# Performance work log

Measured on AMD Instinct MI355X. Metric: run time of the kernel, lower is better.

The kernel has to match this reference:

```python
import jax, jax.numpy as jnp
import numpy as np

MODES = 20
WIDTH = 64
EPS = 1e-5


def spectral_conv(x, w1, w2, m1, m2):
    # x: [B, C, H, W] real; w1, w2: [Ci, Co, m1, m2, 2] (real/imag)
    B, C, H, W = x.shape
    xf = jnp.fft.rfft2(x, norm='ortho')  # [B, C, H, W//2+1] complex
    w1c = w1[..., 0] + 1j * w1[..., 1]
    w2c = w2[..., 0] + 1j * w2[..., 1]
    m1 = min(m1, H)
    m2 = min(m2, W // 2 + 1)
    top = jnp.einsum('bixy,ioxy->boxy', xf[:, :, :m1, :m2], w1c[:, :, :m1, :m2])
    bot = jnp.einsum('bixy,ioxy->boxy', xf[:, :, -m1:, :m2], w2c[:, :, :m1, :m2])
    out = jnp.zeros((B, w1.shape[1], H, W // 2 + 1), dtype=xf.dtype)
    out = out.at[:, :, :m1, :m2].set(top)
    out = out.at[:, :, H - m1:, :m2].set(bot)
    return jnp.fft.irfft2(out, s=(H, W), norm='ortho')


def batchnorm2d(x, gamma, beta):
    # training-mode BN over (B, H, W) per channel; x: [B, C, H, W]
    mean = jnp.mean(x, axis=(0, 2, 3), keepdims=True)
    var = jnp.var(x, axis=(0, 2, 3), keepdims=True)
    xn = (x - mean) * jax.lax.rsqrt(var + EPS)
    return xn * gamma[None, :, None, None] + beta[None, :, None, None]


def setup_inputs() -> dict:
    key = jax.random.key(0)
    ks = jax.random.split(key, 12)
    B, H, W, Tin2 = 8, 256, 256, 12
    scale = 1.0 / (WIDTH * WIDTH)
    return {
        'x': jax.random.normal(ks[0], (B, H, W, Tin2), jnp.float32),
        'fc0_w': jax.random.normal(ks[1], (Tin2, WIDTH), jnp.float32) * 0.1,
        'fc0_b': jnp.zeros((WIDTH,), jnp.float32),
        'sw1': scale * jax.random.normal(ks[2], (4, WIDTH, WIDTH, MODES, MODES, 2), jnp.float32),
        'sw2': scale * jax.random.normal(ks[3], (4, WIDTH, WIDTH, MODES, MODES, 2), jnp.float32),
        'cw': jax.random.normal(ks[4], (4, WIDTH, WIDTH), jnp.float32) * 0.1,
        'cb': jnp.zeros((4, WIDTH), jnp.float32),
        'bng': jnp.ones((4, WIDTH), jnp.float32),
        'bnb': jnp.zeros((4, WIDTH), jnp.float32),
        'fc1_w': jax.random.normal(ks[5], (WIDTH, 128), jnp.float32) * 0.1,
        'fc1_b': jnp.zeros((128,), jnp.float32),
        'fc2_w': jax.random.normal(ks[6], (128, 1), jnp.float32) * 0.1,
        'fc2_b': jnp.zeros((1,), jnp.float32),
    }


def reference(x, fc0_w, fc0_b, sw1, sw2, cw, cb, bng, bnb, fc1_w, fc1_b, fc2_w, fc2_b):
    # lift: [B, H, W, Tin+2] -> [B, C, H, W]
    h = jnp.einsum('bhwt,tc->bhwc', x, fc0_w) + fc0_b
    h = jnp.transpose(h, (0, 3, 1, 2))
    for l in range(4):
        spec = spectral_conv(h, sw1[l], sw2[l], MODES, MODES)
        lin = jnp.einsum('bihw,oi->bohw', h, cw[l]) + cb[l][None, :, None, None]
        h = batchnorm2d(spec + lin, bng[l], bnb[l])
        if l < 3:
            h = jax.nn.relu(h)
    h = jnp.transpose(h, (0, 2, 3, 1))  # [B, H, W, C]
    h = jax.nn.relu(jnp.einsum('bhwc,cd->bhwd', h, fc1_w) + fc1_b)
    out = jnp.einsum('bhwd,de->bhwe', h, fc2_w) + fc2_b
    return out
```

## Files before the change

### kernel.cpp

```cpp
#include <hip/hip_runtime.h>
#include <hip/hip_bf16.h>


__device__ __forceinline__ void gll16(const float* gsrc, float* ldst) {
    __builtin_amdgcn_global_load_lds(
        (const __attribute__((address_space(1))) void*)gsrc,
        (__attribute__((address_space(3))) void*)ldst, 16, 0, 0);
}

__global__ __launch_bounds__(256) void init_k(const float* __restrict__ cw,
                                              float* __restrict__ costab, float* __restrict__ sintab,
                                              float* __restrict__ EAt, float* __restrict__ Tw,
                                              float* __restrict__ cwT, float* __restrict__ stats) {
    int idx = blockIdx.x * 256 + threadIdx.x;
    const float PH = 6.28318530717958647692f / 256.f;
    if (idx < 256) {
        float s, c; sincosf(idx * PH, &s, &c);
        costab[idx] = c; sintab[idx] = s;
    } else if (idx < 256 + 10240) {
        int e = idx - 256;
        int n = e >> 8, w = e & 255, ky = n >> 1;
        int r = (ky * w) & 255;
        float s, c; sincosf(r * PH, &s, &c);
        EAt[e] = (n & 1) ? -s : c;
    } else if (idx < 256 + 20480) {
        int e = idx - 10496;
        int kp = e >> 8, w = e & 255;
        int ky = kp >> 1, p = kp & 1;
        int r = (ky * w) & 255;
        float s, c; sincosf(r * PH, &s, &c);
        float v;
        if (ky == 0) v = p ? 0.f : (1.f / 16.f);
        else         v = p ? (-2.f / 16.f) * s : (2.f / 16.f) * c;
        Tw[e] = v;
    } else if (idx < 256 + 20480 + 16384) {
        int e = idx - 20736;
        int l = e >> 12, r2 = e & 4095;
        int i = r2 >> 6, o = r2 & 63;
        cwT[e] = cw[(l << 12) + (o << 6) + i];
    } else if (idx < 256 + 20480 + 16384 + 2048) {
        stats[idx - 37120] = 0.f;
    }
}

__global__ __launch_bounds__(256) void wtrans_k(const float* __restrict__ sw1,
                                                const float* __restrict__ sw2,
                                                unsigned int* __restrict__ wt) {
    int gid = blockIdx.x * 4 + (threadIdx.x >> 6);
    int o = threadIdx.x & 63;
    int xyc = gid % 25;
    int i = (gid / 25) & 63;
    int t2 = gid / 1600;
    const float* src = ((t2 & 1) ? sw2 : sw1) + (t2 >> 1) * 3276800;
    const float* sp = src + ((i * 64 + o) * 400 + xyc * 16) * 2;
    unsigned int* dp = wt + (size_t)(t2 * 400 + xyc * 16) * 4096 + i * 64 + o;
#pragma unroll
    for (int j = 0; j < 16; ++j) {
        float re = sp[2 * j], im = sp[2 * j + 1];
        unsigned int ur = __float_as_uint(re), ui = __float_as_uint(im);
        ur = (ur + 0x7fffu + ((ur >> 16) & 1u)) >> 16;
        ui = (ui + 0x7fffu + ((ui >> 16) & 1u)) & 0xffff0000u;
        dp[(size_t)j * 4096] = ur | ui;
    }
}

__global__ __launch_bounds__(256) void fc0_k(const float* __restrict__ x,
                                             const float* __restrict__ w,
                                             const float* __restrict__ bias,
                                             float* __restrict__ outb) {
    __shared__ float ws[768];
    __shared__ float bs[64];
    int tid = threadIdx.x;
    for (int i = tid; i < 768; i += 256) ws[i] = w[i];
    if (tid < 64) bs[tid] = bias[tid];
    __syncthreads();
    int pix = blockIdx.x * 256 + tid;
    int b = pix >> 16, hw = pix & 65535;
    float xv[12];
#pragma unroll
    for (int t = 0; t < 12; ++t) xv[t] = x[pix * 12 + t];
    int base = (b << 22) + hw;
    for (int c = 0; c < 64; ++c) {
        float a = bs[c];
#pragma unroll
        for (int t = 0; t < 12; ++t) a += xv[t] * ws[t * 64 + c];
        outb[base + (c << 16)] = a;
    }
}

__global__ __launch_bounds__(128) void dftw_k(float* __restrict__ X,
                                              const float* __restrict__ EAt,
                                              float* __restrict__ T,
                                              const float* __restrict__ statsl,
                                              const float* __restrict__ g,
                                              const float* __restrict__ bt,
                                              int fuse) {
    __shared__ __align__(16) float Xs[32 * 68];
    __shared__ __align__(16) float Est[40 * 32];
    int tid = threadIdx.x;
    int tm = tid >> 3, tn = tid & 7;
    int row0 = blockIdx.x << 6;
    float sc = 1.f, sh = 0.f;
    if (fuse) {
        int c = (row0 >> 8) & 63;
        float ssum = statsl[c] + statsl[128 + c] + statsl[256 + c] + statsl[384 + c];
        float ssq  = statsl[64 + c] + statsl[192 + c] + statsl[320 + c] + statsl[448 + c];
        float mean = ssum * (1.f / 524288.f);
        float var = ssq * (1.f / 524288.f) - mean * mean;
        sc = g[c] * rsqrtf(var + 1e-5f);
        sh = bt[c] - mean * sc;
    }
    float acc[4][5];
#pragma unroll
    for (int i = 0; i < 4; ++i)
#pragma unroll
        for (int j = 0; j < 5; ++j) acc[i][j] = 0.f;

#pragma unroll 1
    for (int kc = 0; kc < 256; kc += 32) {
        __syncthreads();
#pragma unroll
        for (int r = 0; r < 4; ++r) {
            int m = tm + (r << 4);
            float4 v = *(const float4*)&X[(row0 + m) * 256 + kc + (tn << 2)];
            if (fuse) {
                v.x = fmaxf(fmaf(v.x, sc, sh), 0.f);
                v.y = fmaxf(fmaf(v.y, sc, sh), 0.f);
                v.z = fmaxf(fmaf(v.z, sc, sh), 0.f);
                v.w = fmaxf(fmaf(v.w, sc, sh), 0.f);
                *(float4*)&X[(row0 + m) * 256 + kc + (tn << 2)] = v;
            }
            int kb = tn << 2;
            Xs[(kb + 0) * 68 + m] = v.x;
            Xs[(kb + 1) * 68 + m] = v.y;
            Xs[(kb + 2) * 68 + m] = v.z;
            Xs[(kb + 3) * 68 + m] = v.w;
        }
        for (int i = tid; i < 1280; i += 128) Est[i] = EAt[((i >> 5) << 8) + kc + (i & 31)];
        __syncthreads();
#pragma unroll 1
        for (int k4 = 0; k4 < 8; ++k4) {
            float4 e0 = *(const float4*)&Est[(tn * 5 + 0) * 32 + (k4 << 2)];
            float4 e1 = *(const float4*)&Est[(tn * 5 + 1) * 32 + (k4 << 2)];
            float4 e2 = *(const float4*)&Est[(tn * 5 + 2) * 32 + (k4 << 2)];
            float4 e3 = *(const float4*)&Est[(tn * 5 + 3) * 32 + (k4 << 2)];
            float4 e4 = *(const float4*)&Est[(tn * 5 + 4) * 32 + (k4 << 2)];
#pragma unroll
            for (int c2 = 0; c2 < 4; ++c2) {
                float4 a = *(const float4*)&Xs[((k4 << 2) + c2) * 68 + (tm << 2)];
                float ev0 = ((const float*)&e0)[c2];
                float ev1 = ((const float*)&e1)[c2];
                float ev2 = ((const float*)&e2)[c2];
                float ev3 = ((const float*)&e3)[c2];
                float ev4 = ((const float*)&e4)[c2];
                acc[0][0] += a.x * ev0; acc[1][0] += a.y * ev0; acc[2][0] += a.z * ev0; acc[3][0] += a.w * ev0;
                acc[0][1] += a.x * ev1; acc[1][1] += a.y * ev1; acc[2][1] += a.z * ev1; acc[3][1] += a.w * ev1;
                acc[0][2] += a.x * ev2; acc[1][2] += a.y * ev2; acc[2][2] += a.z * ev2; acc[3][2] += a.w * ev2;
                acc[0][3] += a.x * ev3; acc[1][3] += a.y * ev3; acc[2][3] += a.z * ev3; acc[3][3] += a.w * ev3;
                acc[0][4] += a.x * ev4; acc[1][4] += a.y * ev4; acc[2][4] += a.z * ev4; acc[3][4] += a.w * ev4;
            }
        }
    }
#pragma unroll
    for (int i = 0; i < 4; ++i) {
        int row = row0 + (tm << 2) + i;
#pragma unroll
        for (int j = 0; j < 5; ++j) T[row * 40 + tn * 5 + j] = acc[i][j];
    }
}

__global__ __launch_bounds__(256) void dfth_k(const float* __restrict__ T,
                                              const float* __restrict__ ct, const float* __restrict__ st,
                                              float* __restrict__ XF) {
    __shared__ __align__(16) float Ts[10240];
    __shared__ float cts[256], sts[256];
    int tid = threadIdx.x;
    int bc = blockIdx.x;
    for (int i = tid; i < 10240; i += 256) Ts[i] = T[bc * 10240 + i];
    cts[tid] = ct[tid]; sts[tid] = st[tid];
    __syncthreads();
    if (tid < 200) {
        int kxi = tid / 5, kyg = tid % 5;
        int kxa = kxi < 20 ? kxi : kxi + 216;
        float ar0 = 0, ai0 = 0, ar1 = 0, ai1 = 0, ar2 = 0, ai2 = 0, ar3 = 0, ai3 = 0;
        int r = 0;
#pragma unroll 1
        for (int h = 0; h < 256; ++h) {
            float cc = cts[r], sv = sts[r];
            r = (r + kxa) & 255;
            float4 v0 = *(const float4*)&Ts[h * 40 + (kyg << 3)];
            float4 v1 = *(const float4*)&Ts[h * 40 + (kyg << 3) + 4];
            ar0 += v0.x * cc + v0.y * sv;  ai0 += v0.y * cc - v0.x * sv;
            ar1 += v0.z * cc + v0.w * sv;  ai1 += v0.w * cc - v0.z * sv;
            ar2 += v1.x * cc + v1.y * sv;  ai2 += v1.y * cc - v1.x * sv;
            ar3 += v1.z * cc + v1.w * sv;  ai3 += v1.w * cc - v1.z * sv;
        }
        int b = bc >> 6, c = bc & 63;
        const float s = 1.f / 256.f;
        int A = (b * 40 + kxi) * 20 + (kyg << 2);
        float2* O = (float2*)XF;
        O[(A + 0) * 64 + c] = make_float2(ar0 * s, ai0 * s);
        O[(A + 1) * 64 + c] = make_float2(ar1 * s, ai1 * s);
        O[(A + 2) * 64 + c] = make_float2(ar2 * s, ai2 * s);
        O[(A + 3) * 64 + c] = make_float2(ar3 * s, ai3 * s);
    }
}

__global__ __launch_bounds__(512) void eins_t_k(const float* __restrict__ XF,
                                                const unsigned int* __restrict__ wtl,
                                                float* __restrict__ YF) {
    __shared__ float xfs[1024];
    int tid = threadIdx.x;
    int x = blockIdx.x / 20, y = blockIdx.x % 20;
    for (int i = tid; i < 1024; i += 512) {
        int b = i >> 7, rr = i & 127;
        xfs[i] = XF[(b * 40 + x) * 2560 + y * 128 + rr];
    }
    __syncthreads();
    int b = tid >> 6, o = tid & 63;
    const unsigned int* wp = wtl + (size_t)(((x < 20 ? 0 : 400) + (x % 20) * 20 + y)) * 4096 + o;
    float ar = 0.f, ai = 0.f;
#pragma unroll 8
    for (int i = 0; i < 64; ++i) {
        unsigned int wv = wp[i << 6];
        float wr = __uint_as_float(wv << 16);
        float wi = __uint_as_float(wv & 0xffff0000u);
        float xr = xfs[(b << 7) + (i << 1)];
        float xi = xfs[(b << 7) + (i << 1) + 1];
        ar += xr * wr - xi * wi;
        ai += xr * wi + xi * wr;
    }
    ((float2*)YF)[((b * 40 + x) * 20 + y) * 64 + o] = make_float2(ar, ai);
}

__global__ __launch_bounds__(512) void eins_k(const float* __restrict__ XF,
                                              const float* __restrict__ w1, const float* __restrict__ w2,
                                              float* __restrict__ YF) {
    __shared__ float xfs[1024];
    int tid = threadIdx.x;
    int x = blockIdx.x / 20, y = blockIdx.x % 20;
    for (int i = tid; i < 1024; i += 512) {
        int b = i >> 7, rr = i & 127;
        xfs[i] = XF[(b * 40 + x) * 2560 + y * 128 + rr];
    }
    __syncthreads();
    int b = tid >> 6, o = tid & 63;
    const float* wp = (x < 20) ? (w1 + (x * 20 + y) * 2) : (w2 + ((x - 20) * 20 + y) * 2);
    float ar = 0.f, ai = 0.f;
#pragma unroll 8
    for (int i = 0; i < 64; ++i) {
        float2 wv = *(const float2*)&wp[(i * 64 + o) * 800];
        float xr = xfs[(b << 7) + (i << 1)];
        float xi = xfs[(b << 7) + (i << 1) + 1];
        ar += xr * wv.x - xi * wv.y;
        ai += xr * wv.y + xi * wv.x;
    }
    ((float2*)YF)[((b * 40 + x) * 20 + y) * 64 + o] = make_float2(ar, ai);
}

__global__ __launch_bounds__(256) void idfth_k(const float* __restrict__ YF,
                                               const float* __restrict__ ct, const float* __restrict__ st,
                                               float* __restrict__ Z) {
    __shared__ __align__(16) float yfs[1600];
    __shared__ float cts[256], sts[256];
    int tid = threadIdx.x;
    int bc = blockIdx.x;
    int b = bc >> 6, co = bc & 63;
    for (int i = tid; i < 800; i += 256) {
        int kx = i / 20, ky = i % 20;
        float2 v = ((const float2*)YF)[((b * 40 + kx) * 20 + ky) * 64 + co];
        yfs[kx * 40 + 2 * ky] = v.x;
        yfs[kx * 40 + 2 * ky + 1] = v.y;
    }
    cts[tid] = ct[tid]; sts[tid] = st[tid];
    __syncthreads();
    int h = tid;
    float accr[20], acci[20];
#pragma unroll
    for (int q = 0; q < 20; ++q) { accr[q] = 0.f; acci[q] = 0.f; }
#pragma unroll 1
    for (int kxi = 0; kxi < 40; ++kxi) {
        int kxa = kxi < 20 ? kxi : kxi + 216;
        int r = (kxa * h) & 255;
        float cc = cts[r], sv = sts[r];
#pragma unroll
        for (int q = 0; q < 10; ++q) {
            float4 v = *(const float4*)&yfs[kxi * 40 + (q << 2)];
            accr[2 * q]     += v.x * cc - v.y * sv;  acci[2 * q]     += v.x * sv + v.y * cc;
            accr[2 * q + 1] += v.z * cc - v.w * sv;  acci[2 * q + 1] += v.z * sv + v.w * cc;
        }
    }
    const float s = 1.f / 16.f;
    int base = (bc * 256 + h) * 40;
#pragma unroll
    for (int q = 0; q < 10; ++q) {
        float4 o4;
        o4.x = accr[2 * q] * s;     o4.y = acci[2 * q] * s;
        o4.z = accr[2 * q + 1] * s; o4.w = acci[2 * q + 1] * s;
        *(float4*)&Z[base + (q << 2)] = o4;
    }
}

#define FMA2(I, AV, J, B4) \
    acc[I][J].x += (AV) * B4.x; acc[I][J].y += (AV) * B4.y; \
    acc[I][J].z += (AV) * B4.z; acc[I][J].w += (AV) * B4.w;

#define FMA_COL(J, B4) \
    FMA2(0, a0.x, J, B4) FMA2(1, a0.y, J, B4) FMA2(2, a0.z, J, B4) FMA2(3, a0.w, J, B4) \
    FMA2(4, a1.x, J, B4) FMA2(5, a1.y, J, B4) FMA2(6, a1.z, J, B4) FMA2(7, a1.w, J, B4)

#define FMA_COLU(J, B4) \
    FMA2(0, au0.x, J, B4) FMA2(1, au0.y, J, B4) FMA2(2, au0.z, J, B4) FMA2(3, au0.w, J, B4) \
    FMA2(4, au1.x, J, B4) FMA2(5, au1.y, J, B4) FMA2(6, au1.z, J, B4) FMA2(7, au1.w, J, B4)

#define FMA_COLD(J, B4) \
    FMA2(0, ad0.x, J, B4) FMA2(1, ad0.y, J, B4) FMA2(2, ad0.z, J, B4) FMA2(3, ad0.w, J, B4) \
    FMA2(4, ad1.x, J, B4) FMA2(5, ad1.y, J, B4) FMA2(6, ad1.z, J, B4) FMA2(7, ad1.w, J, B4)

__global__ __launch_bounds__(256) void speclin_k(const float* __restrict__ hin,
                                                 const float* __restrict__ Z,
                                                 const float* __restrict__ cwTl,
                                                 const float* __restrict__ Tw,
                                                 const float* __restrict__ cbl,
                                                 float* __restrict__ pre,
                                                 float* __restrict__ statsl) {
    __shared__ __align__(16) float As[64 * 68];
    __shared__ __align__(16) float Zs[80 * 64];
    __shared__ __align__(16) float Bs[2][4096];
    int tid = threadIdx.x;
    int bid = blockIdx.x;
    int b = bid >> 7, hp = bid & 127;
    int h0 = hp << 1;
    int to = tid >> 5, tw = tid & 31;
    int o0 = to << 3;

#pragma unroll
    for (int t = 0; t < 4; ++t) {
        int i4 = tid + (t << 8);
        float4 v = *(const float4*)&cwTl[i4 << 2];
        float* d = &As[(i4 >> 4) * 68 + ((i4 & 15) << 2)];
        d[0] = v.x; d[1] = v.y; d[2] = v.z; d[3] = v.w;
    }
#pragma unroll
    for (int t = 0; t < 5; ++t) {
        int i4 = tid + (t << 8);
        int q = i4 % 10;
        int u = i4 / 10;
        int o = u & 63, r = u >> 6;
        float4 v = *(const float4*)&Z[(((b << 6) + o) * 256 + h0 + r) * 40 + (q << 2)];
        int base = ((r * 40 + (q << 2)) << 6) + o;
        Zs[base]       = v.x;
        Zs[base + 64]  = v.y;
        Zs[base + 128] = v.z;
        Zs[base + 192] = v.w;
    }
    const float* hrow = hin + (size_t)((((b << 6) << 8) + h0) << 8);
#pragma unroll
    for (int t = 0; t < 4; ++t) {
        int i4 = tid + (t << 8);
        int k = i4 >> 7, n4 = i4 & 127, r = n4 >> 6, w4 = n4 & 63;
        gll16(&hrow[(k << 16) + (r << 8) + (w4 << 2)], &Bs[0][i4 << 2]);
    }
    __syncthreads();

    float4 acc[8][4];
#pragma unroll
    for (int i = 0; i < 8; ++i)
#pragma unroll
        for (int j = 0; j < 4; ++j) acc[i][j] = make_float4(0.f, 0.f, 0.f, 0.f);

    int cur = 0;
#pragma unroll 1
    for (int ch = 0; ch < 8; ++ch) {
        if (ch < 7) {
#pragma unroll
            for (int t = 0; t < 4; ++t) {
                int i4 = tid + (t << 8);
                int k = i4 >> 7, n4 = i4 & 127, r = n4 >> 6, w4 = n4 & 63;
                gll16(&hrow[((((ch + 1) << 3) + k) << 16) + (r << 8) + (w4 << 2)],
                      &Bs[cur ^ 1][i4 << 2]);
            }
        } else {
#pragma unroll
            for (int t = 0; t < 2; ++t) {
                int i4 = tid + (t << 8);
                gll16(&Tw[i4 << 2], &Bs[cur ^ 1][i4 << 2]);
            }
        }
        const float* Bc = Bs[cur];
        const float* Ac = &As[(ch << 3) * 68 + o0];
#pragma unroll 1
        for (int kk = 0; kk < 8; ++kk) {
            float4 a0 = *(const float4*)&Ac[kk * 68];
            float4 a1 = *(const float4*)&Ac[kk * 68 + 4];
            float4 b0 = *(const float4*)&Bc[(kk << 9) + (tw << 2)];
            float4 b1 = *(const float4*)&Bc[(kk << 9) + 128 + (tw << 2)];
            FMA_COL(0, b0)
            FMA_COL(1, b1)
            float4 b2 = *(const float4*)&Bc[(kk << 9) + 256 + (tw << 2)];
            float4 b3 = *(const float4*)&Bc[(kk << 9) + 384 + (tw << 2)];
            FMA_COL(2, b2)
            FMA_COL(3, b3)
        }
        __syncthreads();
        cur ^= 1;
    }

#pragma unroll 1
    for (int ch = 0; ch < 5; ++ch) {
        if (ch < 4) {
#pragma unroll
            for (int t = 0; t < 2; ++t) {
                int i4 = tid + (t << 8);
                gll16(&Tw[(((ch + 1) << 3) << 8) + (i4 << 2)], &Bs[cur ^ 1][i4 << 2]);
            }
        }
        const float* Bc = Bs[cur];
#pragma unroll 1
        for (int kk = 0; kk < 8; ++kk) {
            int kp = (ch << 3) + kk;
            float4 b0 = *(const float4*)&Bc[(kk << 8) + (tw << 2)];
            float4 b1 = *(const float4*)&Bc[(kk << 8) + 128 + (tw << 2)];
            float4 au0 = *(const float4*)&Zs[(kp << 6) + o0];
            float4 au1 = *(const float4*)&Zs[(kp << 6) + o0 + 4];
            FMA_COLU(0, b0)
            FMA_COLU(1, b1)
            float4 ad0 = *(const float4*)&Zs[((40 + kp) << 6) + o0];
            float4 ad1 = *(const float4*)&Zs[((40 + kp) << 6) + o0 + 4];
            FMA_COLD(2, b0)
            FMA_COLD(3, b1)
        }
        __syncthreads();
        cur ^= 1;
    }

    float* srep = statsl + ((bid & 3) << 7);
#pragma unroll
    for (int i = 0; i < 8; ++i) {
        float cbv = cbl[o0 + i];
        float sum = 0.f, sq = 0.f;
#pragma unroll
        for (int j = 0; j < 4; ++j) {
            float4 v = acc[i][j];
            v.x += cbv; v.y += cbv; v.z += cbv; v.w += cbv;
            int row = h0 + (j >> 1);
            int wc = ((j & 1) << 7) + (tw << 2);
            *(float4*)&pre[(size_t)((((b << 6) + o0 + i) << 8) + row) * 256 + wc] = v;
            sum += v.x + v.y + v.z + v.w;
            sq  += v.x * v.x + v.y * v.y + v.z * v.z + v.w * v.w;
        }
        sum += __shfl_xor(sum, 1);  sq += __shfl_xor(sq, 1);
        sum += __shfl_xor(sum, 2);  sq += __shfl_xor(sq, 2);
        sum += __shfl_xor(sum, 4);  sq += __shfl_xor(sq, 4);
        sum += __shfl_xor(sum, 8);  sq += __shfl_xor(sq, 8);
        sum += __shfl_xor(sum, 16); sq += __shfl_xor(sq, 16);
        if ((tid & 31) == 0) {
            atomicAdd(&srep[o0 + i], sum);
            atomicAdd(&srep[64 + o0 + i], sq);
        }
    }
}

__global__ __launch_bounds__(256, 2) void fc12_k(const float* __restrict__ hin,
                                                 const float* __restrict__ statsl,
                                                 const float* __restrict__ g,
                                                 const float* __restrict__ bt,
                                                 const float* __restrict__ w1, const float* __restrict__ b1,
                                                 const float* __restrict__ w2, const float* __restrict__ b2,
                                                 float* __restrict__ out) {
    __shared__ __align__(16) float As[64 * 128];
    __shared__ __align__(16) float Bs[2][2048];
    __shared__ float scs[64], shs[64], bias2[128];
    __shared__ __align__(16) float red[4 * 256];
    int tid = threadIdx.x;
    int bh = blockIdx.x;
    int b = bh >> 8, h = bh & 255;
    int to = tid >> 4, tw = tid & 15;
    int d0 = to << 3;

    if (tid < 64) {
        float ssum = statsl[tid] + statsl[128 + tid] + statsl[256 + tid] + statsl[384 + tid];
        float ssq  = statsl[64 + tid] + statsl[192 + tid] + statsl[320 + tid] + statsl[448 + tid];
        float mean = ssum * (1.f / 524288.f);
        float var = ssq * (1.f / 524288.f) - mean * mean;
        float s = g[tid] * rsqrtf(var + 1e-5f);
        scs[tid] = s; shs[tid] = bt[tid] - mean * s;
    }
    __syncthreads();
    for (int i = tid; i < 8192; i += 256) As[i] = w1[i] * scs[i >> 7];
    if (tid < 128) {
        float a = b1[tid];
        for (int c = 0; c < 64; ++c) a += shs[c] * w1[c * 128 + tid];
        bias2[tid] = a;
    }
    const float* hrow = hin + ((size_t)(((b << 6) << 8) + h) << 8);
#pragma unroll
    for (int t = 0; t < 2; ++t) {
        int i4 = tid + (t << 8);
        gll16(&hrow[((i4 >> 6) << 16) + ((i4 & 63) << 2)], &Bs[0][i4 << 2]);
    }
    __syncthreads();

    float4 acc[8][4];
#pragma unroll
    for (int i = 0; i < 8; ++i)
#pragma unroll
        for (int j = 0; j < 4; ++j) acc[i][j] = make_float4(0.f, 0.f, 0.f, 0.f);

    int cur = 0;
#pragma unroll 1
    for (int ch = 0; ch < 8; ++ch) {
        if (ch < 7) {
#pragma unroll
            for (int t = 0; t < 2; ++t) {
                int i4 = tid + (t << 8);
                int k = i4 >> 6, w4 = (i4 & 63) << 2;
                gll16(&hrow[((((ch + 1) << 3) + k) << 16) + w4], &Bs[cur ^ 1][i4 << 2]);
            }
        }
        const float* Bc = Bs[cur];
#pragma unroll 2
        for (int kk = 0; kk < 8; ++kk) {
            int gk = (ch << 3) + kk;
            float4 a0 = *(const float4*)&As[(gk << 7) + d0];
            float4 a1 = *(const float4*)&As[(gk << 7) + d0 + 4];
            float4 b0 = *(const float4*)&Bc[(kk << 8) + (tw << 2)];
            float4 b1 = *(const float4*)&Bc[(kk << 8) + 64 + (tw << 2)];
            FMA_COL(0, b0)
            FMA_COL(1, b1)
            float4 b2 = *(const float4*)&Bc[(kk << 8) + 128 + (tw << 2)];
            float4 b3 = *(const float4*)&Bc[(kk << 8) + 192 + (tw << 2)];
            FMA_COL(2, b2)
            FMA_COL(3, b3)
        }
        __syncthreads();
        cur ^= 1;
    }

    float bb[8], wv[8];
#pragma unroll
    for (int i = 0; i < 8; ++i) { bb[i] = bias2[d0 + i]; wv[i] = w2[d0 + i]; }
    float4 p[4];
#pragma unroll
    for (int j = 0; j < 4; ++j) {
        float4 v = make_float4(0.f, 0.f, 0.f, 0.f);
#pragma unroll
        for (int i = 0; i < 8; ++i) {
            v.x += fmaxf(acc[i][j].x + bb[i], 0.f) * wv[i];
            v.y += fmaxf(acc[i][j].y + bb[i], 0.f) * wv[i];
            v.z += fmaxf(acc[i][j].z + bb[i], 0.f) * wv[i];
            v.w += fmaxf(acc[i][j].w + bb[i], 0.f) * wv[i];
        }
        v.x += __shfl_xor(v.x, 16); v.y += __shfl_xor(v.y, 16);
        v.z += __shfl_xor(v.z, 16); v.w += __shfl_xor(v.w, 16);
        v.x += __shfl_xor(v.x, 32); v.y += __shfl_xor(v.y, 32);
        v.z += __shfl_xor(v.z, 32); v.w += __shfl_xor(v.w, 32);
        p[j] = v;
    }
    int wave = tid >> 6;
    if ((tid & 63) < 16) {
#pragma unroll
        for (int j = 0; j < 4; ++j)
            *(float4*)&red[(wave << 8) + (j << 6) + (tw << 2)] = p[j];
    }
    __syncthreads();
    float s2 = b2[0] + red[tid] + red[256 + tid] + red[512 + tid] + red[768 + tid];
    out[(b * 256 + h) * 256 + tid] = s2;
}

extern "C" void kernel_launch(void* const* d_in, const int* in_sizes, int n_in,
                              void* d_out, int out_size, void* d_ws, size_t ws_size,
                              hipStream_t stream) {
    (void)in_sizes; (void)n_in; (void)out_size;
    const float* x     = (const float*)d_in[0];
    const float* fc0_w = (const float*)d_in[1];
    const float* fc0_b = (const float*)d_in[2];
    const float* sw1   = (const float*)d_in[3];
    const float* sw2   = (const float*)d_in[4];
    const float* cw    = (const float*)d_in[5];
    const float* cb    = (const float*)d_in[6];
    const float* bng   = (const float*)d_in[7];
    const float* bnb   = (const float*)d_in[8];
    const float* fc1_w = (const float*)d_in[9];
    const float* fc1_b = (const float*)d_in[10];
    const float* fc2_w = (const float*)d_in[11];
    const float* fc2_b = (const float*)d_in[12];
    float* out = (float*)d_out;

    float* ws = (float*)d_ws;
    float* hbuf   = ws;
    float* tz     = hbuf + 33554432;
    float* xf     = tz + 5242880;
    float* yf     = xf + 819200;
    float* costab = yf + 819200;
    float* sintab = costab + 256;
    float* EAt    = sintab + 256;
    float* Tw     = EAt + 10240;
    float* cwT    = Tw + 10240;
    float* stats  = cwT + 16384;
    unsigned int* wt = (unsigned int*)(stats + 2048);

    size_t base_floats = 40473600 + 2048;
    int use_wt = (ws_size >= (base_floats + 13107200ull) * 4ull) ? 1 : 0;

    init_k<<<153, 256, 0, stream>>>(cw, costab, sintab, EAt, Tw, cwT, stats);
    if (use_wt) wtrans_k<<<3200, 256, 0, stream>>>(sw1, sw2, wt);
    fc0_k<<<2048, 256, 0, stream>>>(x, fc0_w, fc0_b, hbuf);

    for (int l = 0; l < 4; ++l) {
        if (l == 0)
            dftw_k<<<2048, 128, 0, stream>>>(hbuf, EAt, tz, stats, bng, bnb, 0);
        else
            dftw_k<<<2048, 128, 0, stream>>>(hbuf, EAt, tz, stats + (l - 1) * 512,
                                             bng + (l - 1) * 64, bnb + (l - 1) * 64, 1);
        dfth_k<<<512, 256, 0, stream>>>(tz, costab, sintab, xf);
        if (use_wt)
            eins_t_k<<<800, 512, 0, stream>>>(xf, wt + (size_t)l * 2 * 400 * 4096, yf);
        else
            eins_k<<<800, 512, 0, stream>>>(xf, sw1 + l * 3276800, sw2 + l * 3276800, yf);
        idfth_k<<<512, 256, 0, stream>>>(yf, costab, sintab, tz);
        speclin_k<<<1024, 256, 0, stream>>>(hbuf, tz, cwT + l * 4096, Tw, cb + l * 64,
                                            hbuf, stats + l * 512);
    }
    fc12_k<<<2048, 256, 0, stream>>>(hbuf, stats + 3 * 512, bng + 3 * 64, bnb + 3 * 64,
                                     fc1_w, fc1_b, fc2_w, fc2_b, out);
}
```

Before: 1.229 ms.

## Fuse BN+ReLU into speclin, drop dftw writeback, stage B operand as bf16

The DFT-along-width kernel no longer writes the normalized, ReLU'd activations back to global memory. Instead the spectral+linear kernel recomputes BN scale/shift from the stats and applies BN and ReLU on load. That kernel is retiled to one image row per block. Its input rows and the inverse-DFT twiddle table are now stored in LDS as packed bf16 and unpacked to fp32 for the FMAs, which halves LDS footprint and traffic. The cost is lower precision in the pointwise-conv and twiddle operands, and a different register/LDS balance.

```diff
diff --git a/kernel.cpp b/kernel.cpp
--- a/kernel.cpp
+++ b/kernel.cpp
@@ -8,10 +8,20 @@
         (__attribute__((address_space(3))) void*)ldst, 16, 0, 0);
 }
 
+__device__ __forceinline__ unsigned bfp(float x) {
+    unsigned u = __float_as_uint(x);
+    return (u + 0x7fffu + ((u >> 16) & 1u)) >> 16;
+}
+
+#define UNPK(U, B4) \
+    B4.x = __uint_as_float((U).x << 16); B4.y = __uint_as_float((U).x & 0xffff0000u); \
+    B4.z = __uint_as_float((U).y << 16); B4.w = __uint_as_float((U).y & 0xffff0000u);
+
 __global__ __launch_bounds__(256) void init_k(const float* __restrict__ cw,
                                               float* __restrict__ costab, float* __restrict__ sintab,
                                               float* __restrict__ EAt, float* __restrict__ Tw,
-                                              float* __restrict__ cwT, float* __restrict__ stats) {
+                                              float* __restrict__ cwT, float* __restrict__ stats,
+                                              unsigned* __restrict__ Twh) {
     int idx = blockIdx.x * 256 + threadIdx.x;
     const float PH = 6.28318530717958647692f / 256.f;
     if (idx < 256) {
@@ -40,6 +50,23 @@
         cwT[e] = cw[(l << 12) + (o << 6) + i];
     } else if (idx < 256 + 20480 + 16384 + 2048) {
         stats[idx - 37120] = 0.f;
+    } else if (idx < 256 + 20480 + 16384 + 2048 + 5120) {
+        int e = idx - 39168;
+        int kp = e >> 7, w2 = e & 127;
+        int ky = kp >> 1, p = kp & 1;
+        float v0, v1;
+        {
+            int w = w2 << 1;
+            int r = (ky * w) & 255;
+            float s, c; sincosf(r * PH, &s, &c);
+            v0 = (ky == 0) ? (p ? 0.f : (1.f / 16.f))
+                           : (p ? (-2.f / 16.f) * s : (2.f / 16.f) * c);
+            r = (ky * (w + 1)) & 255;
+            sincosf(r * PH, &s, &c);
+            v1 = (ky == 0) ? (p ? 0.f : (1.f / 16.f))
+                           : (p ? (-2.f / 16.f) * s : (2.f / 16.f) * c);
+        }
+        Twh[e] = bfp(v0) | (bfp(v1) << 16);
     }
 }
 
@@ -57,10 +84,7 @@
 #pragma unroll
     for (int j = 0; j < 16; ++j) {
         float re = sp[2 * j], im = sp[2 * j + 1];
-        unsigned int ur = __float_as_uint(re), ui = __float_as_uint(im);
-        ur = (ur + 0x7fffu + ((ur >> 16) & 1u)) >> 16;
-        ui = (ui + 0x7fffu + ((ui >> 16) & 1u)) & 0xffff0000u;
-        dp[(size_t)j * 4096] = ur | ui;
+        dp[(size_t)j * 4096] = bfp(re) | (bfp(im) << 16);
     }
 }
 
@@ -88,7 +112,7 @@
     }
 }
 
-__global__ __launch_bounds__(128) void dftw_k(float* __restrict__ X,
+__global__ __launch_bounds__(128) void dftw_k(const float* __restrict__ X,
                                               const float* __restrict__ EAt,
                                               float* __restrict__ T,
                                               const float* __restrict__ statsl,
@@ -128,7 +152,6 @@
                 v.y = fmaxf(fmaf(v.y, sc, sh), 0.f);
                 v.z = fmaxf(fmaf(v.z, sc, sh), 0.f);
                 v.w = fmaxf(fmaf(v.w, sc, sh), 0.f);
-                *(float4*)&X[(row0 + m) * 256 + kc + (tn << 2)] = v;
             }
             int kb = tn << 2;
             Xs[(kb + 0) * 68 + m] = v.x;
@@ -309,98 +332,137 @@
     FMA2(0, a0.x, J, B4) FMA2(1, a0.y, J, B4) FMA2(2, a0.z, J, B4) FMA2(3, a0.w, J, B4) \
     FMA2(4, a1.x, J, B4) FMA2(5, a1.y, J, B4) FMA2(6, a1.z, J, B4) FMA2(7, a1.w, J, B4)
 
-#define FMA_COLU(J, B4) \
-    FMA2(0, au0.x, J, B4) FMA2(1, au0.y, J, B4) FMA2(2, au0.z, J, B4) FMA2(3, au0.w, J, B4) \
-    FMA2(4, au1.x, J, B4) FMA2(5, au1.y, J, B4) FMA2(6, au1.z, J, B4) FMA2(7, au1.w, J, B4)
-
-#define FMA_COLD(J, B4) \
-    FMA2(0, ad0.x, J, B4) FMA2(1, ad0.y, J, B4) FMA2(2, ad0.z, J, B4) FMA2(3, ad0.w, J, B4) \
-    FMA2(4, ad1.x, J, B4) FMA2(5, ad1.y, J, B4) FMA2(6, ad1.z, J, B4) FMA2(7, ad1.w, J, B4)
-
 __global__ __launch_bounds__(256) void speclin_k(const float* __restrict__ hin,
                                                  const float* __restrict__ Z,
                                                  const float* __restrict__ cwTl,
-                                                 const float* __restrict__ Tw,
+                                                 const unsigned* __restrict__ Twh,
                                                  const float* __restrict__ cbl,
                                                  float* __restrict__ pre,
-                                                 float* __restrict__ statsl) {
-    __shared__ __align__(16) float As[64 * 68];
-    __shared__ __align__(16) float Zs[80 * 64];
-    __shared__ __align__(16) float Bs[2][4096];
-    int tid = threadIdx.x;
-    int bid = blockIdx.x;
-    int b = bid >> 7, hp = bid & 127;
-    int h0 = hp << 1;
+                                                 float* __restrict__ statsl,
+                                                 const float* __restrict__ statsp,
+                                                 const float* __restrict__ gp,
+                                                 const float* __restrict__ btp,
+                                                 int fuse) {
+    __shared__ __align__(16) float AZ[104 * 64];
+    __shared__ __align__(16) unsigned short BsH[2][2048];
+    __shared__ float scs[64], shs[64];
+    int tid = threadIdx.x;
+    int bh = blockIdx.x;
+    int b = bh >> 8, h = bh & 255;
     int to = tid >> 5, tw = tid & 31;
     int o0 = to << 3;
 
+    if (tid < 64) {
+        float s = 1.f, so = 0.f;
+        if (fuse) {
+            float ssum = statsp[tid] + statsp[128 + tid] + statsp[256 + tid] + statsp[384 + tid];
+            float ssq  = statsp[64 + tid] + statsp[192 + tid] + statsp[320 + tid] + statsp[448 + tid];
+            float mean = ssum * (1.f / 524288.f);
+            float var = ssq * (1.f / 524288.f) - mean * mean;
+            s = gp[tid] * rsqrtf(var + 1e-5f);
+            so = btp[tid] - mean * s;
+        }
+        scs[tid] = s; shs[tid] = so;
+    }
 #pragma unroll
     for (int t = 0; t < 4; ++t) {
         int i4 = tid + (t << 8);
-        float4 v = *(const float4*)&cwTl[i4 << 2];
-        float* d = &As[(i4 >> 4) * 68 + ((i4 & 15) << 2)];
-        d[0] = v.x; d[1] = v.y; d[2] = v.z; d[3] = v.w;
-    }
-#pragma unroll
-    for (int t = 0; t < 5; ++t) {
+        gll16(&cwTl[i4 << 2], &AZ[i4 << 2]);
+    }
+    {
+        const float* Zrow = Z + ((size_t)(((b << 6) << 8) + h)) * 40;
+#pragma unroll
+        for (int t = 0; t < 3; ++t) {
+            int i4 = tid + (t << 8);
+            if (i4 < 640) {
+                int q = i4 % 10, o = i4 / 10;
+                float4 v = *(const float4*)&Zrow[o * 10240 + (q << 2)];
+                int rb = ((64 + (q << 2)) << 6) + o;
+                AZ[rb] = v.x; AZ[rb + 64] = v.y; AZ[rb + 128] = v.z; AZ[rb + 192] = v.w;
+            }
+        }
+    }
+    const float* hrow = hin + ((size_t)(((b << 6) << 8) + h) << 8);
+    float4 st[2];
+#pragma unroll
+    for (int t = 0; t < 2; ++t) {
         int i4 = tid + (t << 8);
-        int q = i4 % 10;
-        int u = i4 / 10;
-        int o = u & 63, r = u >> 6;
-        float4 v = *(const float4*)&Z[(((b << 6) + o) * 256 + h0 + r) * 40 + (q << 2)];
-        int base = ((r * 40 + (q << 2)) << 6) + o;
-        Zs[base]       = v.x;
-        Zs[base + 64]  = v.y;
-        Zs[base + 128] = v.z;
-        Zs[base + 192] = v.w;
-    }
-    const float* hrow = hin + (size_t)((((b << 6) << 8) + h0) << 8);
-#pragma unroll
-    for (int t = 0; t < 4; ++t) {
+        st[t] = *(const float4*)&hrow[((i4 >> 6) << 16) + ((i4 & 63) << 2)];
+    }
+    __syncthreads();
+#pragma unroll
+    for (int t = 0; t < 2; ++t) {
         int i4 = tid + (t << 8);
-        int k = i4 >> 7, n4 = i4 & 127, r = n4 >> 6, w4 = n4 & 63;
-        gll16(&hrow[(k << 16) + (r << 8) + (w4 << 2)], &Bs[0][i4 << 2]);
-    }
-    __syncthreads();
-
-    float4 acc[8][4];
-#pragma unroll
-    for (int i = 0; i < 8; ++i)
-#pragma unroll
-        for (int j = 0; j < 4; ++j) acc[i][j] = make_float4(0.f, 0.f, 0.f, 0.f);
+        int k = i4 >> 6, w4 = i4 & 63;
+        float4 v = st[t];
+        if (fuse) {
+            float sck = scs[k], shk = shs[k];
+            v.x = fmaxf(fmaf(v.x, sck, shk), 0.f);
+            v.y = fmaxf(fmaf(v.y, sck, shk), 0.f);
+            v.z = fmaxf(fmaf(v.z, sck, shk), 0.f);
+            v.w = fmaxf(fmaf(v.w, sck, shk), 0.f);
+        }
+        uint2 u = make_uint2(bfp(v.x) | (bfp(v.y) << 16), bfp(v.z) | (bfp(v.w) << 16));
+        *(uint2*)&BsH[0][(k << 8) + (w4 << 2)] = u;
+    }
+    __syncthreads();
+
+    float4 acc[8][2];
+#pragma unroll
+    for (int i = 0; i < 8; ++i) {
+        acc[i][0] = make_float4(0.f, 0.f, 0.f, 0.f);
+        acc[i][1] = make_float4(0.f, 0.f, 0.f, 0.f);
+    }
 
     int cur = 0;
+    uint2 stw[2];
 #pragma unroll 1
     for (int ch = 0; ch < 8; ++ch) {
         if (ch < 7) {
 #pragma unroll
-            for (int t = 0; t < 4; ++t) {
+            for (int t = 0; t < 2; ++t) {
                 int i4 = tid + (t << 8);
-                int k = i4 >> 7, n4 = i4 & 127, r = n4 >> 6, w4 = n4 & 63;
-                gll16(&hrow[((((ch + 1) << 3) + k) << 16) + (r << 8) + (w4 << 2)],
-                      &Bs[cur ^ 1][i4 << 2]);
+                st[t] = *(const float4*)&hrow[((((ch + 1) << 3) + (i4 >> 6)) << 16) + ((i4 & 63) << 2)];
             }
         } else {
 #pragma unroll
+            for (int t = 0; t < 2; ++t)
+                stw[t] = *(const uint2*)&Twh[(t << 9) + (tid << 1)];
+        }
+        const unsigned short* Bc = BsH[cur];
+        const float* Ac = &AZ[((ch << 3) << 6) + o0];
+#pragma unroll 2
+        for (int kk = 0; kk < 8; ++kk) {
+            float4 a0 = *(const float4*)&Ac[(kk << 6)];
+            float4 a1 = *(const float4*)&Ac[(kk << 6) + 4];
+            uint2 u0 = *(const uint2*)&Bc[(kk << 8) + (tw << 2)];
+            uint2 u1 = *(const uint2*)&Bc[(kk << 8) + 128 + (tw << 2)];
+            float4 b0, b1;
+            UNPK(u0, b0)
+            UNPK(u1, b1)
+            FMA_COL(0, b0)
+            FMA_COL(1, b1)
+        }
+        if (ch < 7) {
+#pragma unroll
             for (int t = 0; t < 2; ++t) {
                 int i4 = tid + (t << 8);
-                gll16(&Tw[i4 << 2], &Bs[cur ^ 1][i4 << 2]);
+                int k = i4 >> 6, w4 = i4 & 63;
+                float4 v = st[t];
+                if (fuse) {
+                    float sck = scs[((ch + 1) << 3) + k], shk = shs[((ch + 1) << 3) + k];
+                    v.x = fmaxf(fmaf(v.x, sck, shk), 0.f);
+                    v.y = fmaxf(fmaf(v.y, sck, shk), 0.f);
+                    v.z = fmaxf(fmaf(v.z, sck, shk), 0.f);
+                    v.w = fmaxf(fmaf(v.w, sck, shk), 0.f);
+                }
+                uint2 u = make_uint2(bfp(v.x) | (bfp(v.y) << 16), bfp(v.z) | (bfp(v.w) << 16));
+                *(uint2*)&BsH[cur ^ 1][(k << 8) + (w4 << 2)] = u;
             }
-        }
-        const float* Bc = Bs[cur];
-        const float* Ac = &As[(ch << 3) * 68 + o0];
-#pragma unroll 1
-        for (int kk = 0; kk < 8; ++kk) {
-            float4 a0 = *(const float4*)&Ac[kk * 68];
-            float4 a1 = *(const float4*)&Ac[kk * 68 + 4];
-            float4 b0 = *(const float4*)&Bc[(kk << 9) + (tw << 2)];
-            float4 b1 = *(const float4*)&Bc[(kk << 9) + 128 + (tw << 2)];
-            FMA_COL(0, b0)
-            FMA_COL(1, b1)
-            float4 b2 = *(const float4*)&Bc[(kk << 9) + 256 + (tw << 2)];
-            float4 b3 = *(const float4*)&Bc[(kk << 9) + 384 + (tw << 2)];
-            FMA_COL(2, b2)
-            FMA_COL(3, b3)
+        } else {
+#pragma unroll
+            for (int t = 0; t < 2; ++t)
+                *(uint2*)&BsH[cur ^ 1][(((t << 9) + (tid << 1)) << 1)] = stw[t];
         }
         __syncthreads();
         cur ^= 1;
@@ -410,42 +472,43 @@
     for (int ch = 0; ch < 5; ++ch) {
         if (ch < 4) {
 #pragma unroll
-            for (int t = 0; t < 2; ++t) {
-                int i4 = tid + (t << 8);
-                gll16(&Tw[(((ch + 1) << 3) << 8) + (i4 << 2)], &Bs[cur ^ 1][i4 << 2]);
-            }
-        }
-        const float* Bc = Bs[cur];
-#pragma unroll 1
+            for (int t = 0; t < 2; ++t)
+                stw[t] = *(const uint2*)&Twh[((ch + 1) << 10) + (t << 9) + (tid << 1)];
+        }
+        const unsigned short* Bc = BsH[cur];
+        const float* Ac = &AZ[(((ch << 3) + 64) << 6) + o0];
+#pragma unroll 2
         for (int kk = 0; kk < 8; ++kk) {
-            int kp = (ch << 3) + kk;
-            float4 b0 = *(const float4*)&Bc[(kk << 8) + (tw << 2)];
-            float4 b1 = *(const float4*)&Bc[(kk << 8) + 128 + (tw << 2)];
-            float4 au0 = *(const float4*)&Zs[(kp << 6) + o0];
-            float4 au1 = *(const float4*)&Zs[(kp << 6) + o0 + 4];
-            FMA_COLU(0, b0)
-            FMA_COLU(1, b1)
-            float4 ad0 = *(const float4*)&Zs[((40 + kp) << 6) + o0];
-            float4 ad1 = *(const float4*)&Zs[((40 + kp) << 6) + o0 + 4];
-            FMA_COLD(2, b0)
-            FMA_COLD(3, b1)
+            float4 a0 = *(const float4*)&Ac[(kk << 6)];
+            float4 a1 = *(const float4*)&Ac[(kk << 6) + 4];
+            uint2 u0 = *(const uint2*)&Bc[(kk << 8) + (tw << 2)];
+            uint2 u1 = *(const uint2*)&Bc[(kk << 8) + 128 + (tw << 2)];
+            float4 b0, b1;
+            UNPK(u0, b0)
+            UNPK(u1, b1)
+            FMA_COL(0, b0)
+            FMA_COL(1, b1)
+        }
+        if (ch < 4) {
+#pragma unroll
+            for (int t = 0; t < 2; ++t)
+                *(uint2*)&BsH[cur ^ 1][(((t << 9) + (tid << 1)) << 1)] = stw[t];
         }
         __syncthreads();
         cur ^= 1;
     }
 
-    float* srep = statsl + ((bid & 3) << 7);
+    float* srep = statsl + ((bh & 3) << 7);
 #pragma unroll
     for (int i = 0; i < 8; ++i) {
         float cbv = cbl[o0 + i];
         float sum = 0.f, sq = 0.f;
-#pragma unroll
-        for (int j = 0; j < 4; ++j) {
+        size_t obase = ((size_t)((((b << 6) + o0 + i) << 8) + h) << 8);
+#pragma unroll
+        for (int j = 0; j < 2; ++j) {
             float4 v = acc[i][j];
             v.x += cbv; v.y += cbv; v.z += cbv; v.w += cbv;
-            int row = h0 + (j >> 1);
-            int wc = ((j & 1) << 7) + (tw << 2);
-            *(float4*)&pre[(size_t)((((b << 6) + o0 + i) << 8) + row) * 256 + wc] = v;
+            *(float4*)&pre[obase + (j << 7) + (tw << 2)] = v;
             sum += v.x + v.y + v.z + v.w;
             sq  += v.x * v.x + v.y * v.y + v.z * v.z + v.w * v.w;
         }
@@ -598,12 +661,13 @@
     float* Tw     = EAt + 10240;
     float* cwT    = Tw + 10240;
     float* stats  = cwT + 16384;
-    unsigned int* wt = (unsigned int*)(stats + 2048);
-
-    size_t base_floats = 40473600 + 2048;
+    unsigned* Twh = (unsigned*)(stats + 2048);
+    unsigned* wt  = Twh + 5120;
+
+    size_t base_floats = 40473600 + 2048 + 5120;
     int use_wt = (ws_size >= (base_floats + 13107200ull) * 4ull) ? 1 : 0;
 
-    init_k<<<153, 256, 0, stream>>>(cw, costab, sintab, EAt, Tw, cwT, stats);
+    init_k<<<173, 256, 0, stream>>>(cw, costab, sintab, EAt, Tw, cwT, stats, Twh);
     if (use_wt) wtrans_k<<<3200, 256, 0, stream>>>(sw1, sw2, wt);
     fc0_k<<<2048, 256, 0, stream>>>(x, fc0_w, fc0_b, hbuf);
 
@@ -619,8 +683,12 @@
         else
             eins_k<<<800, 512, 0, stream>>>(xf, sw1 + l * 3276800, sw2 + l * 3276800, yf);
         idfth_k<<<512, 256, 0, stream>>>(yf, costab, sintab, tz);
-        speclin_k<<<1024, 256, 0, stream>>>(hbuf, tz, cwT + l * 4096, Tw, cb + l * 64,
-                                            hbuf, stats + l * 512);
+        speclin_k<<<2048, 256, 0, stream>>>(hbuf, tz, cwT + l * 4096, Twh, cb + l * 64,
+                                            hbuf, stats + l * 512,
+                                            (l == 0) ? stats : stats + (l - 1) * 512,
+                                            bng + (l ? (l - 1) * 64 : 0),
+                                            bnb + (l ? (l - 1) * 64 : 0),
+                                            l ? 1 : 0);
     }
     fc12_k<<<2048, 256, 0, stream>>>(hbuf, stats + 3 * 512, bng + 3 * 64, bnb + 3 * 64,
                                      fc1_w, fc1_b, fc2_w, fc2_b, out);
```

Result: slower. 1.312 ms (+6.8%).
